# Kernel tuning notes

Measured on AMD Instinct MI355X. Metric: run time of the kernel, lower is better.

Reference implementation:

```python
import jax, jax.numpy as jnp
import numpy as np

N_NODES = 100000
N_EDGES = 1250000
D_IN = 64
D_OUT = 64


def setup_inputs() -> dict:
    key = jax.random.key(0)
    k_h, k_e, k_src, k_dst, k_w, k_b = jax.random.split(key, 6)
    h = jax.random.normal(k_h, (N_NODES, D_IN), dtype=jnp.float32)
    e = jax.random.normal(k_e, (N_EDGES, 1), dtype=jnp.float32)
    src = jax.random.randint(k_src, (N_EDGES,), 0, N_NODES, dtype=jnp.int64)
    dst = jax.random.randint(k_dst, (N_EDGES,), 0, N_NODES, dtype=jnp.int64)
    W = jax.random.normal(k_w, (D_OUT, D_IN), dtype=jnp.float32) / np.sqrt(D_IN)
    b = jax.random.normal(k_b, (D_OUT,), dtype=jnp.float32) * 0.01
    return {"h": h, "e": e, "src": src, "dst": dst, "W": W, "b": b}


def reference(h, e, src, dst, W, b):
    # u_mul_e: gather source node features and multiply by edge features [E,1] -> [E,D]
    m = h[src] * e
    # fn.sum('m','ft'): scatter-add messages into destination nodes -> [N,D]
    ft = jax.ops.segment_sum(m, dst, num_segments=N_NODES)
    # nn.Linear(input_dim, output_dim)
    return ft @ W.T + b
```

## Files before the change

### kernel.cpp

```cpp
#include <hip/hip_runtime.h>

#define N_NODES 100000
#define N_EDGES 1250000
#define D 64
#define BUCKET_BITS 6
#define BUCKET_SZ 64
#define NBUCK 1563
#define CAP 1024
#define EPT 8
#define EPB (EPT * 256)
#define BIN_BLOCKS ((N_EDGES + EPB - 1) / EPB)
#define TR_BLOCKS ((N_NODES + 63) / 64)


typedef __attribute__((ext_vector_type(8))) short bf16x8;
typedef __attribute__((ext_vector_type(4))) float f32x4;

__device__ __forceinline__ unsigned bf16_rne(float x) {
    unsigned u = __float_as_uint(x);
    return (u + 0x7FFFu + ((u >> 16) & 1u)) >> 16;
}
__device__ __forceinline__ float bf16_to_f(unsigned short v) {
    return __uint_as_float(((unsigned)v) << 16);
}

__device__ __forceinline__ void bf16_split(float x, short& hi, short& lo) {
    unsigned hb = bf16_rne(x);
    float fh = __uint_as_float(hb << 16);
    hi = (short)hb;
    lo = (short)bf16_rne(x - fh);
}

__global__ __launch_bounds__(256) void transform_kernel(const float* __restrict__ h,
                                                        const float* __restrict__ W,
                                                        unsigned short* __restrict__ g16,
                                                        int* __restrict__ gcursor) {
    __shared__ unsigned short sh[64 * D];

    int t = threadIdx.x;
    int bx = blockIdx.x;
    if (bx < 7) {
        int i = bx * 256 + t;
        if (i < NBUCK) gcursor[i] = 0;
    }

    int lane = t & 63;
    int w = t >> 6;
    int li = lane & 15;
    int lg = lane >> 4;
    int nodebase = bx * 64 + w * 16;

    int arow = nodebase + li;
    if (arow > N_NODES - 1) arow = N_NODES - 1;

    f32x4 acc[4];
#pragma unroll
    for (int nt = 0; nt < 4; ++nt) acc[nt] = (f32x4){0.f, 0.f, 0.f, 0.f};

#pragma unroll
    for (int kk = 0; kk < 2; ++kk) {
        const float* hp = h + (long)arow * D + kk * 32 + lg * 8;
        float4 h0 = *(const float4*)hp;
        float4 h1 = *(const float4*)(hp + 4);
        float av[8] = {h0.x, h0.y, h0.z, h0.w, h1.x, h1.y, h1.z, h1.w};
        bf16x8 ahi, alo;
#pragma unroll
        for (int q = 0; q < 8; ++q) { short a, b; bf16_split(av[q], a, b); ahi[q] = a; alo[q] = b; }

#pragma unroll
        for (int nt = 0; nt < 4; ++nt) {
            const float* wp = W + (nt * 16 + li) * D + kk * 32 + lg * 8;
            float4 w0 = *(const float4*)wp;
            float4 w1 = *(const float4*)(wp + 4);
            float bv[8] = {w0.x, w0.y, w0.z, w0.w, w1.x, w1.y, w1.z, w1.w};
            bf16x8 bhi, blo;
#pragma unroll
            for (int q = 0; q < 8; ++q) { short a, b; bf16_split(bv[q], a, b); bhi[q] = a; blo[q] = b; }

            acc[nt] = __builtin_amdgcn_mfma_f32_16x16x32_bf16(ahi, bhi, acc[nt], 0, 0, 0);
            acc[nt] = __builtin_amdgcn_mfma_f32_16x16x32_bf16(ahi, blo, acc[nt], 0, 0, 0);
            acc[nt] = __builtin_amdgcn_mfma_f32_16x16x32_bf16(alo, bhi, acc[nt], 0, 0, 0);
        }
    }

#pragma unroll
    for (int nt = 0; nt < 4; ++nt) {
#pragma unroll
        for (int r = 0; r < 4; ++r) {
            sh[(w * 16 + lg * 4 + r) * D + nt * 16 + li] = (unsigned short)bf16_rne(acc[nt][r]);
        }
    }
    __syncthreads();

    const uint4* s4 = (const uint4*)sh;
    uint4* g4 = (uint4*)(g16 + (long)bx * 64 * D);
#pragma unroll
    for (int i = t; i < 512; i += 256) {
        int n = bx * 64 + (i >> 3);
        if (n < N_NODES) g4[i] = s4[i];
    }
}

__global__ __launch_bounds__(256) void bin_edges_kernel(const int* __restrict__ src,
                                                        const int* __restrict__ dst,
                                                        const float* __restrict__ e,
                                                        int* __restrict__ gcursor,
                                                        int2* __restrict__ packed) {
    __shared__ int lhist[NBUCK];
    int t = threadIdx.x;
    for (int j = t; j < NBUCK; j += 256) lhist[j] = 0;
    __syncthreads();

    int b[EPT], r[EPT], sv[EPT];
    float ev[EPT];
    int base = blockIdx.x * EPB;
#pragma unroll
    for (int j = 0; j < EPT; ++j) {
        int i = base + j * 256 + t;
        b[j] = -1;
        if (i < N_EDGES) {
            int d = dst[i];
            b[j] = d >> BUCKET_BITS;
            sv[j] = src[i] | ((d & (BUCKET_SZ - 1)) << 20);
            ev[j] = e[i];
            r[j] = atomicAdd(&lhist[b[j]], 1);
        }
    }
    __syncthreads();

    for (int x = t; x < NBUCK; x += 256) {
        int c = lhist[x];
        lhist[x] = (c > 0) ? atomicAdd(&gcursor[x], c) : 0;
    }
    __syncthreads();

#pragma unroll
    for (int j = 0; j < EPT; ++j) {
        if (b[j] >= 0) {
            int pos = lhist[b[j]] + r[j];
            if (pos < CAP) packed[b[j] * CAP + pos] = make_int2(sv[j], __float_as_int(ev[j]));
        }
    }
}

__global__ __launch_bounds__(512) void gather_bucket_kernel(const unsigned short* __restrict__ g16,
                                                            const int2* __restrict__ packed,
                                                            const int* __restrict__ gcursor,
                                                            const float* __restrict__ bias,
                                                            float* __restrict__ out) {
    __shared__ int2 eds[CAP];
    __shared__ int nhist[BUCKET_SZ];
    __shared__ int nbase[BUCKET_SZ];
    __shared__ int ncur[BUCKET_SZ];

    int t = threadIdx.x;
    int bk = blockIdx.x;
    int start = bk * CAP;
    int cnt = gcursor[bk];
    if (cnt > CAP) cnt = CAP;

    if (t < BUCKET_SZ) nhist[t] = 0;
    __syncthreads();

    int2 pa = make_int2(0, 0), pb = pa;
    bool va = t < cnt, vb = t + 512 < cnt;
    if (va) pa = packed[start + t];
    if (vb) pb = packed[start + t + 512];
    if (va) atomicAdd(&nhist[(pa.x >> 20) & (BUCKET_SZ - 1)], 1);
    if (vb) atomicAdd(&nhist[(pb.x >> 20) & (BUCKET_SZ - 1)], 1);
    __syncthreads();

    if (t < BUCKET_SZ) {
        int c = nhist[t];
        int v = c;
#pragma unroll
        for (int off = 1; off < BUCKET_SZ; off <<= 1) {
            int x = __shfl_up(v, off, 64);
            if (t >= off) v += x;
        }
        nbase[t] = v - c;
        ncur[t] = v - c;
    }
    __syncthreads();

    if (va) { int dl = (pa.x >> 20) & (BUCKET_SZ - 1); eds[atomicAdd(&ncur[dl], 1)] = pa; }
    if (vb) { int dl = (pb.x >> 20) & (BUCKET_SZ - 1); eds[atomicAdd(&ncur[dl], 1)] = pb; }
    __syncthreads();

    int w = t >> 6;
    int lane = t & 63;
    float bv = bias[lane];
    for (int jj = 0; jj < 8; ++jj) {
        int n = w * 8 + jj;
        int gn = bk * BUCKET_SZ + n;
        int s = nbase[n];
        int c = nhist[n];
        float acc = bv;
        int k = 0;
        for (; k + 8 <= c; k += 8) {
            int2 q0 = eds[s + k + 0], q1 = eds[s + k + 1];
            int2 q2 = eds[s + k + 2], q3 = eds[s + k + 3];
            int2 q4 = eds[s + k + 4], q5 = eds[s + k + 5];
            int2 q6 = eds[s + k + 6], q7 = eds[s + k + 7];
            float g0 = bf16_to_f(g16[(long)(q0.x & 0xFFFFF) * D + lane]);
            float g1 = bf16_to_f(g16[(long)(q1.x & 0xFFFFF) * D + lane]);
            float g2 = bf16_to_f(g16[(long)(q2.x & 0xFFFFF) * D + lane]);
            float g3 = bf16_to_f(g16[(long)(q3.x & 0xFFFFF) * D + lane]);
            float g4 = bf16_to_f(g16[(long)(q4.x & 0xFFFFF) * D + lane]);
            float g5 = bf16_to_f(g16[(long)(q5.x & 0xFFFFF) * D + lane]);
            float g6 = bf16_to_f(g16[(long)(q6.x & 0xFFFFF) * D + lane]);
            float g7 = bf16_to_f(g16[(long)(q7.x & 0xFFFFF) * D + lane]);
            acc += __int_as_float(q0.y) * g0;
            acc += __int_as_float(q1.y) * g1;
            acc += __int_as_float(q2.y) * g2;
            acc += __int_as_float(q3.y) * g3;
            acc += __int_as_float(q4.y) * g4;
            acc += __int_as_float(q5.y) * g5;
            acc += __int_as_float(q6.y) * g6;
            acc += __int_as_float(q7.y) * g7;
        }
        if (k + 4 <= c) {
            int2 q0 = eds[s + k + 0], q1 = eds[s + k + 1];
            int2 q2 = eds[s + k + 2], q3 = eds[s + k + 3];
            float g0 = bf16_to_f(g16[(long)(q0.x & 0xFFFFF) * D + lane]);
            float g1 = bf16_to_f(g16[(long)(q1.x & 0xFFFFF) * D + lane]);
            float g2 = bf16_to_f(g16[(long)(q2.x & 0xFFFFF) * D + lane]);
            float g3 = bf16_to_f(g16[(long)(q3.x & 0xFFFFF) * D + lane]);
            acc += __int_as_float(q0.y) * g0;
            acc += __int_as_float(q1.y) * g1;
            acc += __int_as_float(q2.y) * g2;
            acc += __int_as_float(q3.y) * g3;
            k += 4;
        }
        for (; k < c; ++k) {
            int2 q = eds[s + k];
            acc += __int_as_float(q.y) * bf16_to_f(g16[(long)(q.x & 0xFFFFF) * D + lane]);
        }
        if (gn < N_NODES) out[(long)gn * D + lane] = acc;
    }
}

extern "C" void kernel_launch(void* const* d_in, const int* in_sizes, int n_in,
                              void* d_out, int out_size, void* d_ws, size_t ws_size,
                              hipStream_t stream) {
    const float* h   = (const float*)d_in[0];
    const float* e   = (const float*)d_in[1];
    const int*   src = (const int*)d_in[2];
    const int*   dst = (const int*)d_in[3];
    const float* W   = (const float*)d_in[4];
    const float* b   = (const float*)d_in[5];
    float* out = (float*)d_out;

    char* ws = (char*)d_ws;
    int2*           packed  = (int2*)          (ws);
    int*            gcursor = (int*)           (ws + 12804096);
    unsigned short* g16     = (unsigned short*)(ws + 12810368);

    transform_kernel<<<TR_BLOCKS, 256, 0, stream>>>(h, W, g16, gcursor);

    bin_edges_kernel<<<BIN_BLOCKS, 256, 0, stream>>>(src, dst, e, gcursor, packed);

    gather_bucket_kernel<<<NBUCK, 512, 0, stream>>>(g16, packed, gcursor, b, out);
}
```

Baseline: 165.7 us.

## Fuse node transform and edge binning into one interleaved launch

Merges the transform and bin-edges kernels into a single launch whose blocks are interleaved (five transform blocks, then two bin blocks, per group of seven) so the compute-bound MFMA work overlaps the memory- and atomic-bound binning. Zeroing the bucket cursors moves out of the kernel into a hipMemsetAsync, because binning blocks can now run at the same time as the blocks that previously cleared the counters. This removes one kernel boundary and its tail, but adds a memset launch and shares one 8 KB shared buffer between both roles, which may affect occupancy.

Measured after the change: 163.7 us. No clear change (-1.2%).

```diff
diff --git a/kernel.cpp b/kernel.cpp
--- a/kernel.cpp
+++ b/kernel.cpp
@@ -11,6 +11,7 @@
 #define EPB (EPT * 256)
 #define BIN_BLOCKS ((N_EDGES + EPB - 1) / EPB)
 #define TR_BLOCKS ((N_NODES + 63) / 64)
+#define FUSED_BLOCKS (TR_BLOCKS + BIN_BLOCKS)
 
 
 typedef __attribute__((ext_vector_type(8))) short bf16x8;
@@ -31,114 +32,116 @@
     lo = (short)bf16_rne(x - fh);
 }
 
-__global__ __launch_bounds__(256) void transform_kernel(const float* __restrict__ h,
-                                                        const float* __restrict__ W,
-                                                        unsigned short* __restrict__ g16,
-                                                        int* __restrict__ gcursor) {
-    __shared__ unsigned short sh[64 * D];
+__global__ __launch_bounds__(256) void transform_bin_kernel(const float* __restrict__ h,
+                                                            const float* __restrict__ W,
+                                                            unsigned short* __restrict__ g16,
+                                                            const int* __restrict__ src,
+                                                            const int* __restrict__ dst,
+                                                            const float* __restrict__ e,
+                                                            int* __restrict__ gcursor,
+                                                            int2* __restrict__ packed) {
+    __shared__ __align__(16) char smem_raw[8192];
 
     int t = threadIdx.x;
     int bx = blockIdx.x;
-    if (bx < 7) {
-        int i = bx * 256 + t;
-        if (i < NBUCK) gcursor[i] = 0;
-    }
-
-    int lane = t & 63;
-    int w = t >> 6;
-    int li = lane & 15;
-    int lg = lane >> 4;
-    int nodebase = bx * 64 + w * 16;
-
-    int arow = nodebase + li;
-    if (arow > N_NODES - 1) arow = N_NODES - 1;
-
-    f32x4 acc[4];
-#pragma unroll
-    for (int nt = 0; nt < 4; ++nt) acc[nt] = (f32x4){0.f, 0.f, 0.f, 0.f};
-
-#pragma unroll
-    for (int kk = 0; kk < 2; ++kk) {
-        const float* hp = h + (long)arow * D + kk * 32 + lg * 8;
-        float4 h0 = *(const float4*)hp;
-        float4 h1 = *(const float4*)(hp + 4);
-        float av[8] = {h0.x, h0.y, h0.z, h0.w, h1.x, h1.y, h1.z, h1.w};
-        bf16x8 ahi, alo;
-#pragma unroll
-        for (int q = 0; q < 8; ++q) { short a, b; bf16_split(av[q], a, b); ahi[q] = a; alo[q] = b; }
+    int g = bx / 7, s = bx % 7;
+    int cand = g * 2 + (s - 5);
+    bool is_bin = (s >= 5) && (cand < BIN_BLOCKS);
+    int nb = g * 2 + ((s == 6) ? 1 : 0);
+    if (nb > BIN_BLOCKS) nb = BIN_BLOCKS;
+
+    if (!is_bin) {
+        unsigned short* sh = (unsigned short*)smem_raw;
+        int trb = bx - nb;
+        int lane = t & 63;
+        int w = t >> 6;
+        int li = lane & 15;
+        int lg = lane >> 4;
+        int nodebase = trb * 64 + w * 16;
+
+        int arow = nodebase + li;
+        if (arow > N_NODES - 1) arow = N_NODES - 1;
+
+        f32x4 acc[4];
+#pragma unroll
+        for (int nt = 0; nt < 4; ++nt) acc[nt] = (f32x4){0.f, 0.f, 0.f, 0.f};
+
+#pragma unroll
+        for (int kk = 0; kk < 2; ++kk) {
+            const float* hp = h + (long)arow * D + kk * 32 + lg * 8;
+            float4 h0 = *(const float4*)hp;
+            float4 h1 = *(const float4*)(hp + 4);
+            float av[8] = {h0.x, h0.y, h0.z, h0.w, h1.x, h1.y, h1.z, h1.w};
+            bf16x8 ahi, alo;
+#pragma unroll
+            for (int q = 0; q < 8; ++q) { short a, b; bf16_split(av[q], a, b); ahi[q] = a; alo[q] = b; }
+
+#pragma unroll
+            for (int nt = 0; nt < 4; ++nt) {
+                const float* wp = W + (nt * 16 + li) * D + kk * 32 + lg * 8;
+                float4 w0 = *(const float4*)wp;
+                float4 w1 = *(const float4*)(wp + 4);
+                float bv[8] = {w0.x, w0.y, w0.z, w0.w, w1.x, w1.y, w1.z, w1.w};
+                bf16x8 bhi, blo;
+#pragma unroll
+                for (int q = 0; q < 8; ++q) { short a, b; bf16_split(bv[q], a, b); bhi[q] = a; blo[q] = b; }
+
+                acc[nt] = __builtin_amdgcn_mfma_f32_16x16x32_bf16(ahi, bhi, acc[nt], 0, 0, 0);
+                acc[nt] = __builtin_amdgcn_mfma_f32_16x16x32_bf16(ahi, blo, acc[nt], 0, 0, 0);
+                acc[nt] = __builtin_amdgcn_mfma_f32_16x16x32_bf16(alo, bhi, acc[nt], 0, 0, 0);
+            }
+        }
 
 #pragma unroll
         for (int nt = 0; nt < 4; ++nt) {
-            const float* wp = W + (nt * 16 + li) * D + kk * 32 + lg * 8;
-            float4 w0 = *(const float4*)wp;
-            float4 w1 = *(const float4*)(wp + 4);
-            float bv[8] = {w0.x, w0.y, w0.z, w0.w, w1.x, w1.y, w1.z, w1.w};
-            bf16x8 bhi, blo;
-#pragma unroll
-            for (int q = 0; q < 8; ++q) { short a, b; bf16_split(bv[q], a, b); bhi[q] = a; blo[q] = b; }
-
-            acc[nt] = __builtin_amdgcn_mfma_f32_16x16x32_bf16(ahi, bhi, acc[nt], 0, 0, 0);
-            acc[nt] = __builtin_amdgcn_mfma_f32_16x16x32_bf16(ahi, blo, acc[nt], 0, 0, 0);
-            acc[nt] = __builtin_amdgcn_mfma_f32_16x16x32_bf16(alo, bhi, acc[nt], 0, 0, 0);
-        }
-    }
-
-#pragma unroll
-    for (int nt = 0; nt < 4; ++nt) {
-#pragma unroll
-        for (int r = 0; r < 4; ++r) {
-            sh[(w * 16 + lg * 4 + r) * D + nt * 16 + li] = (unsigned short)bf16_rne(acc[nt][r]);
-        }
-    }
-    __syncthreads();
-
-    const uint4* s4 = (const uint4*)sh;
-    uint4* g4 = (uint4*)(g16 + (long)bx * 64 * D);
-#pragma unroll
-    for (int i = t; i < 512; i += 256) {
-        int n = bx * 64 + (i >> 3);
-        if (n < N_NODES) g4[i] = s4[i];
-    }
-}
-
-__global__ __launch_bounds__(256) void bin_edges_kernel(const int* __restrict__ src,
-                                                        const int* __restrict__ dst,
-                                                        const float* __restrict__ e,
-                                                        int* __restrict__ gcursor,
-                                                        int2* __restrict__ packed) {
-    __shared__ int lhist[NBUCK];
-    int t = threadIdx.x;
-    for (int j = t; j < NBUCK; j += 256) lhist[j] = 0;
-    __syncthreads();
-
-    int b[EPT], r[EPT], sv[EPT];
-    float ev[EPT];
-    int base = blockIdx.x * EPB;
-#pragma unroll
-    for (int j = 0; j < EPT; ++j) {
-        int i = base + j * 256 + t;
-        b[j] = -1;
-        if (i < N_EDGES) {
-            int d = dst[i];
-            b[j] = d >> BUCKET_BITS;
-            sv[j] = src[i] | ((d & (BUCKET_SZ - 1)) << 20);
-            ev[j] = e[i];
-            r[j] = atomicAdd(&lhist[b[j]], 1);
-        }
-    }
-    __syncthreads();
-
-    for (int x = t; x < NBUCK; x += 256) {
-        int c = lhist[x];
-        lhist[x] = (c > 0) ? atomicAdd(&gcursor[x], c) : 0;
-    }
-    __syncthreads();
-
-#pragma unroll
-    for (int j = 0; j < EPT; ++j) {
-        if (b[j] >= 0) {
-            int pos = lhist[b[j]] + r[j];
-            if (pos < CAP) packed[b[j] * CAP + pos] = make_int2(sv[j], __float_as_int(ev[j]));
+#pragma unroll
+            for (int r = 0; r < 4; ++r) {
+                sh[(w * 16 + lg * 4 + r) * D + nt * 16 + li] = (unsigned short)bf16_rne(acc[nt][r]);
+            }
+        }
+        __syncthreads();
+
+        const uint4* s4 = (const uint4*)sh;
+        uint4* g4 = (uint4*)(g16 + (long)trb * 64 * D);
+#pragma unroll
+        for (int i = t; i < 512; i += 256) {
+            int n = trb * 64 + (i >> 3);
+            if (n < N_NODES) g4[i] = s4[i];
+        }
+    } else {
+        int* lhist = (int*)smem_raw;
+        for (int j = t; j < NBUCK; j += 256) lhist[j] = 0;
+        __syncthreads();
+
+        int b[EPT], r[EPT], sv[EPT];
+        float ev[EPT];
+        int base = cand * EPB;
+#pragma unroll
+        for (int j = 0; j < EPT; ++j) {
+            int i = base + j * 256 + t;
+            b[j] = -1;
+            if (i < N_EDGES) {
+                int d = dst[i];
+                b[j] = d >> BUCKET_BITS;
+                sv[j] = src[i] | ((d & (BUCKET_SZ - 1)) << 20);
+                ev[j] = e[i];
+                r[j] = atomicAdd(&lhist[b[j]], 1);
+            }
+        }
+        __syncthreads();
+
+        for (int x = t; x < NBUCK; x += 256) {
+            int c = lhist[x];
+            lhist[x] = (c > 0) ? atomicAdd(&gcursor[x], c) : 0;
+        }
+        __syncthreads();
+
+#pragma unroll
+        for (int j = 0; j < EPT; ++j) {
+            if (b[j] >= 0) {
+                int pos = lhist[b[j]] + r[j];
+                if (pos < CAP) packed[b[j] * CAP + pos] = make_int2(sv[j], __float_as_int(ev[j]));
+            }
         }
     }
 }
@@ -256,9 +259,9 @@
     int*            gcursor = (int*)           (ws + 12804096);
     unsigned short* g16     = (unsigned short*)(ws + 12810368);
 
-    transform_kernel<<<TR_BLOCKS, 256, 0, stream>>>(h, W, g16, gcursor);
-
-    bin_edges_kernel<<<BIN_BLOCKS, 256, 0, stream>>>(src, dst, e, gcursor, packed);
+    hipMemsetAsync(gcursor, 0, NBUCK * sizeof(int), stream);
+
+    transform_bin_kernel<<<FUSED_BLOCKS, 256, 0, stream>>>(h, W, g16, src, dst, e, gcursor, packed);
 
     gather_bucket_kernel<<<NBUCK, 512, 0, stream>>>(g16, packed, gcursor, b, out);
 }
```
